# Kernel tuning notes

Hardware: AMD Instinct MI355X
Metric: run time of the kernel (lower is better)

The kernel has to match this reference:

```python
import jax, jax.numpy as jnp
import numpy as np

S, B, H = 2048, 32, 1024

def setup_inputs() -> dict:
    key = jax.random.key(0)
    k1, k2, k3 = jax.random.split(key, 3)
    hidden = jax.random.normal(k1, (1, B, H), dtype=jnp.float32)
    encoder_outputs = jax.random.normal(k2, (S, B, H), dtype=jnp.float32)
    W = jax.random.normal(k3, (H, H), dtype=jnp.float32) * (1.0 / np.sqrt(H))
    b = jnp.zeros((H,), dtype=jnp.float32)
    return {"hidden": hidden, "encoder_outputs": encoder_outputs, "W": W, "b": b}

def reference(hidden, encoder_outputs, W, b):
    # method == 'general': energy[b,i] = hidden[0,b] . (W @ enc[i,b] + bias)
    # proj: [S, B, H] = enc @ W^T + b  (nn.Linear convention: y = x W^T + b)
    proj = jnp.einsum('sbh,kh->sbk', encoder_outputs, W) + b
    # scores: [B, S]
    scores = jnp.einsum('bh,sbh->bs', hidden[0], proj)
    attn = jax.nn.softmax(scores, axis=1)
    return attn[:, None, :]  # [B, 1, S]
```

## Files before the change

### kernel.cpp

```cpp
#include <hip/hip_runtime.h>
#include <math.h>

#define H 1024
#define S 2048
#define B 32

__global__ void __launch_bounds__(512)
proj_hidden_kernel(const float* __restrict__ hidden,
                   const float* __restrict__ W,
                   float* __restrict__ v) {
    __shared__ float hs[2][H];
    __shared__ float part[32][2][64];
    const int hc = blockIdx.x & 15;
    const int bg = blockIdx.x >> 4;
    const int hq = threadIdx.x & 15;
    const int kg = threadIdx.x >> 4;

    for (int i = threadIdx.x; i < 2 * H; i += 512)
        hs[i >> 10][i & 1023] = hidden[(bg * 2 + (i >> 10)) * H + (i & 1023)];
    __syncthreads();

    const int h = hc * 64 + hq * 4;
    float4 a0 = {0.f, 0.f, 0.f, 0.f};
    float4 a1 = {0.f, 0.f, 0.f, 0.f};
#pragma unroll 4
    for (int kk = 0; kk < 32; ++kk) {
        const int k = kg + 32 * kk;
        const float h0 = hs[0][k];
        const float h1 = hs[1][k];
        const float4 w = *reinterpret_cast<const float4*>(W + (size_t)k * H + h);
        a0.x = fmaf(h0, w.x, a0.x); a0.y = fmaf(h0, w.y, a0.y);
        a0.z = fmaf(h0, w.z, a0.z); a0.w = fmaf(h0, w.w, a0.w);
        a1.x = fmaf(h1, w.x, a1.x); a1.y = fmaf(h1, w.y, a1.y);
        a1.z = fmaf(h1, w.z, a1.z); a1.w = fmaf(h1, w.w, a1.w);
    }
    *reinterpret_cast<float4*>(&part[kg][0][hq * 4]) = a0;
    *reinterpret_cast<float4*>(&part[kg][1][hq * 4]) = a1;
    __syncthreads();

    if (threadIdx.x < 128) {
        const int bb = threadIdx.x >> 6;
        const int c  = threadIdx.x & 63;
        float sum = 0.f;
#pragma unroll 8
        for (int g = 0; g < 32; ++g) sum += part[g][bb][c];
        v[(bg * 2 + bb) * H + hc * 64 + c] = sum;
    }
}

__global__ void __launch_bounds__(256)
scores_kernel(const float* __restrict__ enc,
              const float* __restrict__ v,
              float* __restrict__ scores) {
    const int s0 = blockIdx.x * 4;
    const int b  = threadIdx.x >> 3;
    const int k  = threadIdx.x & 7;

    const float4* e0 = reinterpret_cast<const float4*>(enc + ((size_t)(s0 + 0) * B + b) * H);
    const float4* e1 = reinterpret_cast<const float4*>(enc + ((size_t)(s0 + 1) * B + b) * H);
    const float4* e2 = reinterpret_cast<const float4*>(enc + ((size_t)(s0 + 2) * B + b) * H);
    const float4* e3 = reinterpret_cast<const float4*>(enc + ((size_t)(s0 + 3) * B + b) * H);
    const float4* vb = reinterpret_cast<const float4*>(v + (size_t)b * H);

    float a0 = 0.f, a1 = 0.f, a2 = 0.f, a3 = 0.f;
#pragma unroll 4
    for (int j = 0; j < 32; ++j) {
        const int f = k + 8 * j;
        const float4 w = vb[f];
        const float4 x0 = e0[f];
        const float4 x1 = e1[f];
        const float4 x2 = e2[f];
        const float4 x3 = e3[f];
        a0 = fmaf(x0.x, w.x, fmaf(x0.y, w.y, fmaf(x0.z, w.z, fmaf(x0.w, w.w, a0))));
        a1 = fmaf(x1.x, w.x, fmaf(x1.y, w.y, fmaf(x1.z, w.z, fmaf(x1.w, w.w, a1))));
        a2 = fmaf(x2.x, w.x, fmaf(x2.y, w.y, fmaf(x2.z, w.z, fmaf(x2.w, w.w, a2))));
        a3 = fmaf(x3.x, w.x, fmaf(x3.y, w.y, fmaf(x3.z, w.z, fmaf(x3.w, w.w, a3))));
    }
#pragma unroll
    for (int off = 4; off > 0; off >>= 1) {
        a0 += __shfl_down(a0, off, 8);
        a1 += __shfl_down(a1, off, 8);
        a2 += __shfl_down(a2, off, 8);
        a3 += __shfl_down(a3, off, 8);
    }
    if (k == 0) {
        float* sp = scores + (size_t)b * S + s0;
        sp[0] = a0; sp[1] = a1; sp[2] = a2; sp[3] = a3;
    }
}

__global__ void __launch_bounds__(256)
softmax_kernel(const float* __restrict__ scores,
               float* __restrict__ out) {
    const int b    = blockIdx.x;
    const int tid  = threadIdx.x;
    const int wave = tid >> 6;
    const int lane = tid & 63;

    __shared__ float wmax[4];
    __shared__ float wsum[4];

    float x[8];
    float m = -INFINITY;
#pragma unroll
    for (int i = 0; i < 8; ++i) {
        x[i] = scores[(size_t)b * S + tid + i * 256];
        m = fmaxf(m, x[i]);
    }
#pragma unroll
    for (int off = 32; off > 0; off >>= 1)
        m = fmaxf(m, __shfl_down(m, off, 64));
    if (lane == 0) wmax[wave] = m;
    __syncthreads();
    m = fmaxf(fmaxf(wmax[0], wmax[1]), fmaxf(wmax[2], wmax[3]));

    float sum = 0.f;
#pragma unroll
    for (int i = 0; i < 8; ++i) {
        x[i] = __expf(x[i] - m);
        sum += x[i];
    }
#pragma unroll
    for (int off = 32; off > 0; off >>= 1)
        sum += __shfl_down(sum, off, 64);
    if (lane == 0) wsum[wave] = sum;
    __syncthreads();
    sum = (wsum[0] + wsum[1]) + (wsum[2] + wsum[3]);

    const float inv = 1.0f / sum;
#pragma unroll
    for (int i = 0; i < 8; ++i) {
        out[(size_t)b * S + tid + i * 256] = x[i] * inv;
    }
}

extern "C" void kernel_launch(void* const* d_in, const int* in_sizes, int n_in,
                              void* d_out, int out_size, void* d_ws, size_t ws_size,
                              hipStream_t stream) {
    const float* hidden = (const float*)d_in[0];
    const float* enc    = (const float*)d_in[1];
    const float* W      = (const float*)d_in[2];

    float* v      = (float*)d_ws;
    float* scores = v + (size_t)B * H;
    float* out    = (float*)d_out;

    proj_hidden_kernel<<<256, 512, 0, stream>>>(hidden, W, v);
    scores_kernel<<<S / 4, 256, 0, stream>>>(enc, v, scores);
    softmax_kernel<<<B, 256, 0, stream>>>(scores, out);
}
```

Before: 54.58 us.

## Remap scores kernel so each wave streams full contiguous encoder rows

Each block now handles one batch index and a strip of 64 sequence positions, and each wave reduces whole 4 KB encoder rows, with lanes reading consecutive float4s. The v vector for the batch is held in registers for the whole block instead of being reloaded per iteration. This targets better coalescing and fewer redundant v reads in the bandwidth-bound pass over the 256 MB encoder tensor. It costs a full 64-lane shuffle reduction per group of four rows and changes the grid shape.

```diff
diff --git a/kernel.cpp b/kernel.cpp
--- a/kernel.cpp
+++ b/kernel.cpp
@@ -52,40 +52,51 @@
 scores_kernel(const float* __restrict__ enc,
               const float* __restrict__ v,
               float* __restrict__ scores) {
-    const int s0 = blockIdx.x * 4;
-    const int b  = threadIdx.x >> 3;
-    const int k  = threadIdx.x & 7;
+    const int b     = blockIdx.x & 31;
+    const int strip = blockIdx.x >> 5;
+    const int wave  = threadIdx.x >> 6;
+    const int lane  = threadIdx.x & 63;
 
-    const float4* e0 = reinterpret_cast<const float4*>(enc + ((size_t)(s0 + 0) * B + b) * H);
-    const float4* e1 = reinterpret_cast<const float4*>(enc + ((size_t)(s0 + 1) * B + b) * H);
-    const float4* e2 = reinterpret_cast<const float4*>(enc + ((size_t)(s0 + 2) * B + b) * H);
-    const float4* e3 = reinterpret_cast<const float4*>(enc + ((size_t)(s0 + 3) * B + b) * H);
     const float4* vb = reinterpret_cast<const float4*>(v + (size_t)b * H);
+    float4 vf0 = vb[lane];
+    float4 vf1 = vb[lane + 64];
+    float4 vf2 = vb[lane + 128];
+    float4 vf3 = vb[lane + 192];
 
-    float a0 = 0.f, a1 = 0.f, a2 = 0.f, a3 = 0.f;
-#pragma unroll 4
-    for (int j = 0; j < 32; ++j) {
-        const int f = k + 8 * j;
-        const float4 w = vb[f];
-        const float4 x0 = e0[f];
-        const float4 x1 = e1[f];
-        const float4 x2 = e2[f];
-        const float4 x3 = e3[f];
-        a0 = fmaf(x0.x, w.x, fmaf(x0.y, w.y, fmaf(x0.z, w.z, fmaf(x0.w, w.w, a0))));
-        a1 = fmaf(x1.x, w.x, fmaf(x1.y, w.y, fmaf(x1.z, w.z, fmaf(x1.w, w.w, a1))));
-        a2 = fmaf(x2.x, w.x, fmaf(x2.y, w.y, fmaf(x2.z, w.z, fmaf(x2.w, w.w, a2))));
-        a3 = fmaf(x3.x, w.x, fmaf(x3.y, w.y, fmaf(x3.z, w.z, fmaf(x3.w, w.w, a3))));
-    }
+    const int s_base = strip * 64 + wave * 16;
+    const float4* enc4 = reinterpret_cast<const float4*>(enc);
+
+    for (int i = 0; i < 16; i += 4) {
+        const int s = s_base + i;
+        const float4* r0 = enc4 + ((size_t)(s + 0) * B + b) * 256;
+        const float4* r1 = enc4 + ((size_t)(s + 1) * B + b) * 256;
+        const float4* r2 = enc4 + ((size_t)(s + 2) * B + b) * 256;
+        const float4* r3 = enc4 + ((size_t)(s + 3) * B + b) * 256;
+
+        float a0 = 0.f, a1 = 0.f, a2 = 0.f, a3 = 0.f;
+#define ROWQ(acc, rp, q, vf)                                            \
+        {                                                               \
+            const float4 e = rp[lane + 64 * q];                         \
+            acc = fmaf(e.x, vf.x, fmaf(e.y, vf.y,                       \
+                  fmaf(e.z, vf.z, fmaf(e.w, vf.w, acc))));              \
+        }
+        ROWQ(a0, r0, 0, vf0) ROWQ(a0, r0, 1, vf1) ROWQ(a0, r0, 2, vf2) ROWQ(a0, r0, 3, vf3)
+        ROWQ(a1, r1, 0, vf0) ROWQ(a1, r1, 1, vf1) ROWQ(a1, r1, 2, vf2) ROWQ(a1, r1, 3, vf3)
+        ROWQ(a2, r2, 0, vf0) ROWQ(a2, r2, 1, vf1) ROWQ(a2, r2, 2, vf2) ROWQ(a2, r2, 3, vf3)
+        ROWQ(a3, r3, 0, vf0) ROWQ(a3, r3, 1, vf1) ROWQ(a3, r3, 2, vf2) ROWQ(a3, r3, 3, vf3)
+#undef ROWQ
+
 #pragma unroll
-    for (int off = 4; off > 0; off >>= 1) {
-        a0 += __shfl_down(a0, off, 8);
-        a1 += __shfl_down(a1, off, 8);
-        a2 += __shfl_down(a2, off, 8);
-        a3 += __shfl_down(a3, off, 8);
-    }
-    if (k == 0) {
-        float* sp = scores + (size_t)b * S + s0;
-        sp[0] = a0; sp[1] = a1; sp[2] = a2; sp[3] = a3;
+        for (int off = 32; off > 0; off >>= 1) {
+            a0 += __shfl_down(a0, off, 64);
+            a1 += __shfl_down(a1, off, 64);
+            a2 += __shfl_down(a2, off, 64);
+            a3 += __shfl_down(a3, off, 64);
+        }
+        if (lane == 0) {
+            float4 r = {a0, a1, a2, a3};
+            *reinterpret_cast<float4*>(scores + (size_t)b * S + s) = r;
+        }
     }
 }
 
@@ -146,6 +157,6 @@
     float* out    = (float*)d_out;
 
     proj_hidden_kernel<<<256, 512, 0, stream>>>(hidden, W, v);
-    scores_kernel<<<S / 4, 256, 0, stream>>>(enc, v, scores);
+    scores_kernel<<<1024, 256, 0, stream>>>(enc, v, scores);
     softmax_kernel<<<B, 256, 0, stream>>>(scores, out);
 }
```

Result: slower. 59.70 us (+9.4%).
